# Performance work log

Hardware: AMD Instinct MI355X
Metric: run time of the kernel (lower is better)

The kernel has to match this reference:

```python
import jax, jax.numpy as jnp
import numpy as np

B, E_DIM, N_EXP, EXP_SZ, N_TASKS, TOPK = 16384, 512, 16, 512, 2, 3
D_IN = 2 * E_DIM      # 1024
D_HID = 4 * E_DIM     # 2048
EPS = 1e-5


def _ln(x, g, b):
    mu = jnp.mean(x, axis=-1, keepdims=True)
    var = jnp.var(x, axis=-1, keepdims=True)
    return (x - mu) * jax.lax.rsqrt(var + EPS) * g + b


def setup_inputs() -> dict:
    key = jax.random.key(0)
    ks = jax.random.split(key, 24)
    def w(k, shape, fan_in):
        return jax.random.normal(k, shape, jnp.float32) * (1.0 / np.sqrt(fan_in))
    return {
        "emb_paper": jax.random.normal(ks[0], (B, E_DIM), jnp.float32),
        "emb_reviewer": jax.random.normal(ks[1], (B, E_DIM), jnp.float32),
        # interaction encoder
        "enc_W1": w(ks[2], (D_IN, D_HID), D_IN), "enc_b1": jnp.zeros((D_HID,), jnp.float32),
        "ln1_g": jnp.ones((D_HID,), jnp.float32), "ln1_b": jnp.zeros((D_HID,), jnp.float32),
        "enc_W2": w(ks[3], (D_HID, D_IN), D_HID), "enc_b2": jnp.zeros((D_IN,), jnp.float32),
        "ln2_g": jnp.ones((D_IN,), jnp.float32), "ln2_b": jnp.zeros((D_IN,), jnp.float32),
        # per-task gates (stacked over task axis)
        "gW1": w(ks[4], (N_TASKS, D_IN, 128), D_IN), "gb1": jnp.zeros((N_TASKS, 128), jnp.float32),
        "gW2": w(ks[5], (N_TASKS, 128, N_EXP), 128), "gb2": jnp.zeros((N_TASKS, N_EXP), jnp.float32),
        # stacked experts
        "We1": w(ks[6], (N_EXP, D_IN, EXP_SZ), D_IN), "be1": jnp.zeros((N_EXP, EXP_SZ), jnp.float32),
        "We2": w(ks[7], (N_EXP, EXP_SZ, EXP_SZ), EXP_SZ), "be2": jnp.zeros((N_EXP, EXP_SZ), jnp.float32),
        # per-task towers
        "tW1": w(ks[8], (N_TASKS, EXP_SZ, 256), EXP_SZ), "tb1": jnp.zeros((N_TASKS, 256), jnp.float32),
        "tW2": w(ks[9], (N_TASKS, 256, 128), 256), "tb2": jnp.zeros((N_TASKS, 128), jnp.float32),
        "tW3": w(ks[10], (N_TASKS, 128, 1), 128), "tb3": jnp.zeros((N_TASKS, 1), jnp.float32),
        "task_idx": 0,
    }


def reference(emb_paper, emb_reviewer, enc_W1, enc_b1, ln1_g, ln1_b, enc_W2, enc_b2,
              ln2_g, ln2_b, gW1, gb1, gW2, gb2, We1, be1, We2, be2,
              tW1, tb1, tW2, tb2, tW3, tb3, task_idx):
    # interaction encoder (eval mode: dropout is identity)
    x = jnp.concatenate([emb_paper, emb_reviewer], axis=-1)          # [B, 2E]
    h = jax.nn.relu(_ln(x @ enc_W1 + enc_b1, ln1_g, ln1_b))          # [B, 4E]
    feat = _ln(h @ enc_W2 + enc_b2, ln2_g, ln2_b)                    # [B, 2E]

    # task gate -> top-k sparse softmax gates (no router noise in eval)
    g = jax.nn.relu(feat @ gW1[task_idx] + gb1[task_idx])
    logits = g @ gW2[task_idx] + gb2[task_idx]                       # [B, E]
    top_s, top_i = jax.lax.top_k(logits, TOPK)                       # [B, k]
    gates = jnp.zeros_like(logits).at[jnp.arange(logits.shape[0])[:, None], top_i].set(
        jax.nn.softmax(top_s, axis=-1))

    # dense expert stack (faithful to original: all experts computed)
    e1 = jax.nn.relu(jnp.einsum('bi,eio->beo', feat, We1) + be1[None])   # [B, E, S]
    eo = jnp.einsum('beo,eoh->beh', e1, We2) + be2[None]                 # [B, E, S]
    mix = jnp.einsum('be,beh->bh', gates, eo)                            # [B, S]

    # task tower
    t = jax.nn.relu(mix @ tW1[task_idx] + tb1[task_idx])
    t = jax.nn.relu(t @ tW2[task_idx] + tb2[task_idx])
    out = jax.nn.sigmoid(t @ tW3[task_idx] + tb3[task_idx]).squeeze(-1)  # [B]
    return out, task_idx, gates
```

## Files before the change

kernel.cpp:

```cpp
#include <hip/hip_runtime.h>

typedef __attribute__((ext_vector_type(8))) _Float16 f16x8;
typedef __attribute__((ext_vector_type(4))) float f32x4;

#define DEVINL __device__ __forceinline__

constexpr int BATCH = 16384;
constexpr int DIN   = 1024;
constexpr int DHID  = 2048;
constexpr int NEXP  = 16;
constexpr int EXPSZ = 512;
constexpr int NPAIR = BATCH * 3;

DEVINL unsigned short f2h(float v) {
  _Float16 h = (_Float16)v;
  return __builtin_bit_cast(unsigned short, h);
}
DEVINL float h2f(unsigned short u) {
  return (float)__builtin_bit_cast(_Float16, u);
}

DEVINL void gl2lds(const unsigned short* src, char* ldst) {
  __builtin_amdgcn_global_load_lds((const __attribute__((address_space(1))) void*)src,
                                   (__attribute__((address_space(3))) void*)ldst, 16, 0, 0);
}

template<int SPLIT, int AMODE, int EPI, int BK, int NYT, int TASK>
__global__ __launch_bounds__(256, SPLIT ? 2 : 3)
void mgemm_k(const unsigned short* __restrict__ A0p,
             const unsigned short* __restrict__ A1p,
             const unsigned short* __restrict__ B0p,
             const unsigned short* __restrict__ B1p,
             const float* __restrict__ biasb,
             float* __restrict__ Cf, unsigned short* __restrict__ Cb0,
             unsigned short* __restrict__ Cb1,
             const int* __restrict__ pairRow, const float* __restrict__ pairW,
             const int* __restrict__ counts, const int* __restrict__ offs,
             const int* __restrict__ taskPtr,
             int M, int N, int K)
{
  constexpr int KG = BK / 8;
  constexpr int UNITS = 128 * KG;
  constexpr int ISS = UNITS / 256;
  constexpr int NKK = BK / 32;
  constexpr int NARR = SPLIT ? 4 : 2;
  constexpr bool EXPERT = (AMODE == 1 || AMODE == 2);
  __shared__ char smem[NARR * UNITS * 16];
  char* sA0 = smem;
  char* sA1 = smem + UNITS * 16;
  char* sB0 = smem + (SPLIT ? 2 : 1) * UNITS * 16;
  char* sB1 = smem + 3 * UNITS * 16;

  int Mloc = M, rowBase = 0;
  const unsigned short* b0 = B0p;
  const unsigned short* b1 = B1p;
  const float* bias = biasb;
  if (EXPERT) {
    const int e = blockIdx.z;
    Mloc = counts[e];
    rowBase = offs[e];
    const size_t eo = (size_t)e * (size_t)K * N;
    b0 = B0p + eo;
    if (SPLIT) b1 = B1p + eo;
    bias = biasb + (size_t)e * N;
  }
  if (TASK) bias = biasb + (size_t)(*taskPtr) * N;

  const int xcd = (int)blockIdx.x & 7;
  const int j   = (int)blockIdx.x >> 3;
  const int tile0 = (xcd + 8 * (j / NYT)) * 128;
  const int col0  = (j % NYT) * 128;
  if (tile0 >= Mloc) return;

  const int tid = threadIdx.x;
  const int lane = tid & 63;
  const int wr = ((tid >> 6) >> 1) * 64;
  const int wc = ((tid >> 6) & 1) * 64;
  const int l15 = lane & 15;
  const int lg = lane >> 4;

  const int srow = tid & 127;
  size_t aoff;
  if (AMODE == 0) {
    aoff = (size_t)(tile0 + srow) * K;
  } else if (AMODE == 1) {
    int p = rowBase + tile0 + srow; p = p < NPAIR - 1 ? p : NPAIR - 1;
    aoff = (size_t)pairRow[p] * K;
  } else {
    int p = rowBase + tile0 + srow; p = p < NPAIR - 1 ? p : NPAIR - 1;
    aoff = (size_t)p * K;
  }
  const size_t boff = (size_t)(col0 + srow) * K;

  f32x4 acc[4][4];
  f32x4 acc2[4][4];
  #pragma unroll
  for (int m = 0; m < 4; ++m)
    #pragma unroll
    for (int n = 0; n < 4; ++n) {
      acc[m][n] = f32x4{0.f, 0.f, 0.f, 0.f};
      if (SPLIT) acc2[m][n] = f32x4{0.f, 0.f, 0.f, 0.f};
    }

  for (int kt = 0; kt < K; kt += BK) {
    #pragma unroll
    for (int it = 0; it < ISS; ++it) {
      const int uo = (it * 256 + (tid & 192)) * 16;
      const int ko = kt + (it * 2 + (tid >> 7)) * 8;
      gl2lds(A0p + aoff + ko, sA0 + uo);
      if (SPLIT) gl2lds(A1p + aoff + ko, sA1 + uo);
      gl2lds(b0 + boff + ko, sB0 + uo);
      if (SPLIT) gl2lds(b1 + boff + ko, sB1 + uo);
    }
    __syncthreads();
    #pragma unroll
    for (int kk = 0; kk < NKK; ++kk) {
      const int g = kk * 4 + lg;
      f16x8 b0f[4], b1f[4];
      #pragma unroll
      for (int n = 0; n < 4; ++n) {
        const size_t off = (size_t)(g * 128 + wc + n * 16 + l15) * 16;
        b0f[n] = *(const f16x8*)(sB0 + off);
        if (SPLIT) b1f[n] = *(const f16x8*)(sB1 + off);
      }
      #pragma unroll
      for (int m = 0; m < 4; ++m) {
        const size_t ao = (size_t)(g * 128 + wr + m * 16 + l15) * 16;
        const f16x8 a0 = *(const f16x8*)(sA0 + ao);
        f16x8 a1;
        if (SPLIT) a1 = *(const f16x8*)(sA1 + ao);
        #pragma unroll
        for (int n = 0; n < 4; ++n) {
          if (SPLIT) {
            acc2[m][n] = __builtin_amdgcn_mfma_f32_16x16x32_f16(a1, b0f[n], acc2[m][n], 0, 0, 0);
            acc2[m][n] = __builtin_amdgcn_mfma_f32_16x16x32_f16(a0, b1f[n], acc2[m][n], 0, 0, 0);
          }
          acc[m][n] = __builtin_amdgcn_mfma_f32_16x16x32_f16(a0, b0f[n], acc[m][n], 0, 0, 0);
        }
      }
    }
    __syncthreads();
  }

  #pragma unroll
  for (int n = 0; n < 4; ++n) {
    const int cn = col0 + wc + n * 16 + l15;
    const float bv = bias[cn];
    #pragma unroll
    for (int m = 0; m < 4; ++m) {
      const int r0 = wr + m * 16 + ((lane >> 4) << 2);
      #pragma unroll
      for (int jj = 0; jj < 4; ++jj) {
        const int rm = tile0 + r0 + jj;
        if (EXPERT && rm >= Mloc) continue;
        float v = acc[m][n][jj];
        if (SPLIT) v += acc2[m][n][jj] * (1.f / 2048.f);
        v += bv;
        const size_t ci = (size_t)(EXPERT ? (rowBase + rm) : rm) * N + cn;
        if (EPI == 0) {
          const unsigned short h0 = f2h(v);
          Cb0[ci] = h0;
          Cb1[ci] = f2h((v - h2f(h0)) * 2048.f);
        } else if (EPI == 1) {
          Cb0[ci] = f2h(fmaxf(v, 0.f));
        } else if (EPI == 2) {
          Cb0[ci] = f2h(v * pairW[rowBase + rm]);
        } else {
          Cf[ci] = v;
        }
      }
    }
  }
}

template<bool RELU>
__global__ __launch_bounds__(256, 2)
void gemm32_k(const float* __restrict__ Av, const float* __restrict__ Bb,
              const float* __restrict__ biasb, float* __restrict__ Cv,
              const int* __restrict__ taskPtr, int M, int N, int K)
{
  __shared__ float As[16][128];
  __shared__ float Bs[16][128];
  const int t = *taskPtr;
  const float* Bw = Bb + (size_t)t * K * N;
  const float* bias = biasb + (size_t)t * N;
  const int tile0 = blockIdx.x * 128;
  const int col0 = blockIdx.y * 128;
  const int tid = threadIdx.x;
  const int am = tid >> 1, ak = (tid & 1) * 8;
  const int bk = tid >> 4, bn = (tid & 15) * 8;
  const int rg = (tid >> 4) * 8, cg = (tid & 15) * 8;
  const float* aptr = Av + (size_t)(tile0 + am) * K;

  float acc[8][8];
  #pragma unroll
  for (int i = 0; i < 8; ++i)
    #pragma unroll
    for (int j = 0; j < 8; ++j) acc[i][j] = 0.f;

  for (int kt = 0; kt < K; kt += 16) {
    {
      const float* src = aptr + kt + ak;
      float4 x0 = *reinterpret_cast<const float4*>(src);
      float4 x1 = *reinterpret_cast<const float4*>(src + 4);
      As[ak+0][am]=x0.x; As[ak+1][am]=x0.y; As[ak+2][am]=x0.z; As[ak+3][am]=x0.w;
      As[ak+4][am]=x1.x; As[ak+5][am]=x1.y; As[ak+6][am]=x1.z; As[ak+7][am]=x1.w;
    }
    {
      const float* bsrc = Bw + (size_t)(kt + bk) * N + (col0 + bn);
      float4 b0 = *reinterpret_cast<const float4*>(bsrc);
      float4 b1 = *reinterpret_cast<const float4*>(bsrc + 4);
      Bs[bk][bn+0]=b0.x; Bs[bk][bn+1]=b0.y; Bs[bk][bn+2]=b0.z; Bs[bk][bn+3]=b0.w;
      Bs[bk][bn+4]=b1.x; Bs[bk][bn+5]=b1.y; Bs[bk][bn+6]=b1.z; Bs[bk][bn+7]=b1.w;
    }
    __syncthreads();
    #pragma unroll
    for (int k = 0; k < 16; ++k) {
      float4 a0 = *reinterpret_cast<const float4*>(&As[k][rg]);
      float4 a1 = *reinterpret_cast<const float4*>(&As[k][rg + 4]);
      float4 c0 = *reinterpret_cast<const float4*>(&Bs[k][cg]);
      float4 c1 = *reinterpret_cast<const float4*>(&Bs[k][cg + 4]);
      const float a[8] = {a0.x,a0.y,a0.z,a0.w,a1.x,a1.y,a1.z,a1.w};
      const float b[8] = {c0.x,c0.y,c0.z,c0.w,c1.x,c1.y,c1.z,c1.w};
      #pragma unroll
      for (int i = 0; i < 8; ++i)
        #pragma unroll
        for (int j = 0; j < 8; ++j)
          acc[i][j] = fmaf(a[i], b[j], acc[i][j]);
    }
    __syncthreads();
  }
  #pragma unroll
  for (int i = 0; i < 8; ++i) {
    const int mr = tile0 + rg + i;
    #pragma unroll
    for (int j = 0; j < 8; ++j) {
      float v = acc[i][j] + bias[col0 + cg + j];
      if (RELU) v = fmaxf(v, 0.f);
      Cv[(size_t)mr * N + col0 + cg + j] = v;
    }
  }
}

template<int LEV, int TASK>
__global__ __launch_bounds__(256)
void transp_k(const float* __restrict__ src, unsigned short* __restrict__ d0,
              unsigned short* __restrict__ d1, const int* __restrict__ taskPtr,
              int R, int C)
{
  __shared__ float tle[32][33];
  size_t bb = (size_t)blockIdx.z * R * C;
  if (TASK) bb = (size_t)(*taskPtr) * R * C;
  const int r0 = blockIdx.x * 32, c0 = blockIdx.y * 32;
  const int x = threadIdx.x & 31, y = threadIdx.x >> 5;
  #pragma unroll
  for (int i = 0; i < 32; i += 8)
    tle[y + i][x] = src[bb + (size_t)(r0 + y + i) * C + (c0 + x)];
  __syncthreads();
  const size_t db = TASK ? 0 : (size_t)blockIdx.z * R * C;
  #pragma unroll
  for (int i = 0; i < 32; i += 8) {
    const float v = tle[x][y + i];
    const size_t di = db + (size_t)(c0 + y + i) * R + (r0 + x);
    const unsigned short h0 = f2h(v);
    d0[di] = h0;
    if (LEV > 1) d1[di] = f2h((v - h2f(h0)) * 2048.f);
  }
}

__global__ __launch_bounds__(256)
void convx_k(const float* __restrict__ eP, const float* __restrict__ eR,
             unsigned short* __restrict__ x0, unsigned short* __restrict__ x1)
{
  const size_t u = (size_t)blockIdx.x * 256 + threadIdx.x;
  const size_t row = u >> 8;
  const int c4 = (int)(u & 255) * 4;
  const float* s = (c4 < 512) ? (eP + row * 512 + c4) : (eR + row * 512 + (c4 - 512));
  const float4 v = *(const float4*)s;
  const float vv[4] = {v.x, v.y, v.z, v.w};
  ushort4 h4, l4;
  unsigned short* hp = (unsigned short*)&h4;
  unsigned short* lp = (unsigned short*)&l4;
  #pragma unroll
  for (int j = 0; j < 4; ++j) {
    const unsigned short h0 = f2h(vv[j]);
    hp[j] = h0;
    lp[j] = f2h((vv[j] - h2f(h0)) * 2048.f);
  }
  *(ushort4*)(x0 + row * 1024 + c4) = h4;
  *(ushort4*)(x1 + row * 1024 + c4) = l4;
}

template<int COLS, bool RELU>
__global__ __launch_bounds__(256)
void ln_pair_k(unsigned short* __restrict__ h0, unsigned short* __restrict__ h1,
               const float* __restrict__ g, const float* __restrict__ b)
{
  constexpr int PER = COLS / 256;
  const size_t row = blockIdx.x;
  unsigned short* r0 = h0 + row * COLS;
  unsigned short* r1 = h1 + row * COLS;
  const int c0 = threadIdx.x * PER;
  float v[PER];
  float s = 0.f, s2 = 0.f;
  #pragma unroll
  for (int i = 0; i < PER; i += 4) {
    const ushort4 a = *(const ushort4*)(r0 + c0 + i);
    const ushort4 c = *(const ushort4*)(r1 + c0 + i);
    v[i+0] = h2f(a.x) + h2f(c.x) * (1.f/2048.f);
    v[i+1] = h2f(a.y) + h2f(c.y) * (1.f/2048.f);
    v[i+2] = h2f(a.z) + h2f(c.z) * (1.f/2048.f);
    v[i+3] = h2f(a.w) + h2f(c.w) * (1.f/2048.f);
  }
  #pragma unroll
  for (int i = 0; i < PER; ++i) { s += v[i]; s2 += v[i] * v[i]; }
  #pragma unroll
  for (int o = 1; o < 64; o <<= 1) { s += __shfl_xor(s, o); s2 += __shfl_xor(s2, o); }
  __shared__ float ss[4], ss2[4];
  const int w = threadIdx.x >> 6;
  if ((threadIdx.x & 63) == 0) { ss[w] = s; ss2[w] = s2; }
  __syncthreads();
  s  = ss[0] + ss[1] + ss[2] + ss[3];
  s2 = ss2[0] + ss2[1] + ss2[2] + ss2[3];
  const float mu = s * (1.f / COLS);
  const float var = s2 * (1.f / COLS) - mu * mu;
  const float rs = rsqrtf(var + 1e-5f);
  #pragma unroll
  for (int i = 0; i < PER; i += 4) {
    ushort4 a4, c4v;
    unsigned short* ap = (unsigned short*)&a4;
    unsigned short* cp = (unsigned short*)&c4v;
    #pragma unroll
    for (int j = 0; j < 4; ++j) {
      const int c = c0 + i + j;
      float y = (v[i+j] - mu) * rs * g[c] + b[c];
      if (RELU) y = fmaxf(y, 0.f);
      const unsigned short hh = f2h(y);
      ap[j] = hh;
      cp[j] = f2h((y - h2f(hh)) * 2048.f);
    }
    *(ushort4*)(r0 + c0 + i) = a4;
    *(ushort4*)(r1 + c0 + i) = c4v;
  }
}

template<int COLS, bool RELU, bool F16OUT>
__global__ __launch_bounds__(256)
void ln_k(float* __restrict__ x, const float* __restrict__ g, const float* __restrict__ b,
          unsigned short* __restrict__ x16)
{
  constexpr int PER = COLS / 256;
  const size_t row = blockIdx.x;
  float* xr = x + row * COLS;
  float v[PER];
  float s = 0.f, s2 = 0.f;
  #pragma unroll
  for (int i = 0; i < PER; ++i) {
    v[i] = xr[threadIdx.x + i * 256];
    s += v[i];
    s2 += v[i] * v[i];
  }
  #pragma unroll
  for (int o = 1; o < 64; o <<= 1) { s += __shfl_xor(s, o); s2 += __shfl_xor(s2, o); }
  __shared__ float ss[4], ss2[4];
  const int w = threadIdx.x >> 6;
  if ((threadIdx.x & 63) == 0) { ss[w] = s; ss2[w] = s2; }
  __syncthreads();
  s  = ss[0] + ss[1] + ss[2] + ss[3];
  s2 = ss2[0] + ss2[1] + ss2[2] + ss2[3];
  const float mu = s * (1.f / COLS);
  const float var = s2 * (1.f / COLS) - mu * mu;
  const float rs = rsqrtf(var + 1e-5f);
  #pragma unroll
  for (int i = 0; i < PER; ++i) {
    const int c = threadIdx.x + i * 256;
    float y = (v[i] - mu) * rs * g[c] + b[c];
    if (RELU) y = fmaxf(y, 0.f);
    xr[c] = y;
    if (F16OUT) x16[row * COLS + c] = f2h(y);
  }
}

__global__ __launch_bounds__(256)
void gate_topk_k(const float* __restrict__ g, const float* __restrict__ gW2,
                 const float* __restrict__ gb2, const int* __restrict__ taskPtr,
                 float* __restrict__ gatesOut, int* __restrict__ topkIdx,
                 float* __restrict__ topkW)
{
  const int t = *taskPtr;
  const float* W = gW2 + (size_t)t * 128 * 16;
  const float* bias = gb2 + (size_t)t * 16;
  const int lane = threadIdx.x & 63;
  const int row = blockIdx.x * 4 + (threadIdx.x >> 6);
  const float* gr = g + (size_t)row * 128;
  const int e = lane & 15;
  const int q = lane >> 4;
  float s = 0.f;
  for (int j = q * 32; j < q * 32 + 32; ++j) s = fmaf(gr[j], W[j * 16 + e], s);
  s += __shfl_xor(s, 16);
  s += __shfl_xor(s, 32);
  s += bias[e];
  float logits[16];
  #pragma unroll
  for (int i = 0; i < 16; ++i) logits[i] = __shfl(s, i);
  int i0 = 0; float v0 = logits[0];
  #pragma unroll
  for (int i = 1; i < 16; ++i) if (logits[i] > v0) { v0 = logits[i]; i0 = i; }
  int i1 = -1; float v1 = -3.4e38f;
  #pragma unroll
  for (int i = 0; i < 16; ++i) if (i != i0 && logits[i] > v1) { v1 = logits[i]; i1 = i; }
  int i2 = -1; float v2 = -3.4e38f;
  #pragma unroll
  for (int i = 0; i < 16; ++i) if (i != i0 && i != i1 && logits[i] > v2) { v2 = logits[i]; i2 = i; }
  const float ex1 = expf(v1 - v0);
  const float ex2 = expf(v2 - v0);
  const float inv = 1.f / (1.f + ex1 + ex2);
  const float p0 = inv, p1 = ex1 * inv, p2 = ex2 * inv;
  if (lane < 16) {
    const float gv = (lane == i0) ? p0 : (lane == i1) ? p1 : (lane == i2) ? p2 : 0.f;
    gatesOut[(size_t)row * 16 + lane] = gv;
  }
  if (lane == 0) {
    topkIdx[row * 3 + 0] = i0; topkIdx[row * 3 + 1] = i1; topkIdx[row * 3 + 2] = i2;
    topkW [row * 3 + 0] = p0; topkW [row * 3 + 1] = p1; topkW [row * 3 + 2] = p2;
  }
}

__global__ __launch_bounds__(256)
void hist_k(const int* __restrict__ topkIdx, int* __restrict__ chunkCnt)
{
  __shared__ int lc[NEXP];
  if (threadIdx.x < NEXP) lc[threadIdx.x] = 0;
  __syncthreads();
  const int row = blockIdx.x * 256 + threadIdx.x;
  #pragma unroll
  for (int k = 0; k < 3; ++k) atomicAdd(&lc[topkIdx[row * 3 + k]], 1);
  __syncthreads();
  if (threadIdx.x < NEXP) chunkCnt[blockIdx.x * NEXP + threadIdx.x] = lc[threadIdx.x];
}

__global__ void scanB_k(const int* __restrict__ chunkCnt, int* __restrict__ counts,
                        int* __restrict__ offs, int* __restrict__ chunkBase)
{
  if (threadIdx.x == 0) {
    int tot[NEXP];
    for (int e = 0; e < NEXP; ++e) tot[e] = 0;
    for (int c = 0; c < 64; ++c)
      for (int e = 0; e < NEXP; ++e) tot[e] += chunkCnt[c * NEXP + e];
    int a = 0;
    for (int e = 0; e < NEXP; ++e) { offs[e] = a; counts[e] = tot[e]; a += tot[e]; }
    for (int e = 0; e < NEXP; ++e) {
      int b = offs[e];
      for (int c = 0; c < 64; ++c) { chunkBase[c * NEXP + e] = b; b += chunkCnt[c * NEXP + e]; }
    }
  }
}

__global__ __launch_bounds__(256)
void fill2_k(const int* __restrict__ topkIdx, const float* __restrict__ topkW,
             const int* __restrict__ chunkBase, int* __restrict__ pairRow,
             float* __restrict__ pairW, int* __restrict__ rowPos)
{
  __shared__ int lc[NEXP];
  if (threadIdx.x < NEXP) lc[threadIdx.x] = 0;
  __syncthreads();
  const int row = blockIdx.x * 256 + threadIdx.x;
  #pragma unroll
  for (int k = 0; k < 3; ++k) {
    const int e = topkIdx[row * 3 + k];
    const int lofs = atomicAdd(&lc[e], 1);
    const int pos = chunkBase[blockIdx.x * NEXP + e] + lofs;
    pairRow[pos] = row;
    pairW[pos] = topkW[row * 3 + k];
    rowPos[row * 3 + k] = pos;
  }
}

__global__ __launch_bounds__(256)
void mixreduce_k(const unsigned short* __restrict__ eo, const int* __restrict__ rowPos,
                 unsigned short* __restrict__ mix16)
{
  const size_t row = blockIdx.x;
  const size_t p0 = rowPos[row * 3 + 0];
  const size_t p1 = rowPos[row * 3 + 1];
  const size_t p2 = rowPos[row * 3 + 2];
  for (int c = threadIdx.x; c < EXPSZ; c += 256) {
    mix16[row * EXPSZ + c] = f2h(h2f(eo[p0 * EXPSZ + c]) + h2f(eo[p1 * EXPSZ + c])
                               + h2f(eo[p2 * EXPSZ + c]));
  }
}

__global__ __launch_bounds__(256)
void tower3_k(const unsigned short* __restrict__ t2, const float* __restrict__ tW3,
              const float* __restrict__ tb3, const int* __restrict__ taskPtr,
              float* __restrict__ out)
{
  const int t = *taskPtr;
  const float* w = tW3 + (size_t)t * 128;
  const float bias = tb3[t];
  const int lane = threadIdx.x & 63;
  const int row = blockIdx.x * 4 + (threadIdx.x >> 6);
  const unsigned short* x = t2 + (size_t)row * 128;
  float s = fmaf(h2f(x[lane]), w[lane], h2f(x[lane + 64]) * w[lane + 64]);
  #pragma unroll
  for (int o = 1; o < 64; o <<= 1) s += __shfl_xor(s, o);
  if (lane == 0) out[row] = 1.f / (1.f + expf(-(s + bias)));
  if (blockIdx.x == 0 && threadIdx.x == 0) out[BATCH] = (float)t;
}

extern "C" void kernel_launch(void* const* d_in, const int* in_sizes, int n_in,
                              void* d_out, int out_size, void* d_ws, size_t ws_size,
                              hipStream_t stream)
{
  (void)in_sizes; (void)n_in; (void)out_size; (void)ws_size;
  const float* embP  = (const float*)d_in[0];
  const float* embR  = (const float*)d_in[1];
  const float* encW1 = (const float*)d_in[2];
  const float* encB1 = (const float*)d_in[3];
  const float* ln1g  = (const float*)d_in[4];
  const float* ln1b  = (const float*)d_in[5];
  const float* encW2 = (const float*)d_in[6];
  const float* encB2 = (const float*)d_in[7];
  const float* ln2g  = (const float*)d_in[8];
  const float* ln2b  = (const float*)d_in[9];
  const float* gW1   = (const float*)d_in[10];
  const float* gb1   = (const float*)d_in[11];
  const float* gW2   = (const float*)d_in[12];
  const float* gb2   = (const float*)d_in[13];
  const float* We1   = (const float*)d_in[14];
  const float* be1   = (const float*)d_in[15];
  const float* We2   = (const float*)d_in[16];
  const float* be2   = (const float*)d_in[17];
  const float* tW1   = (const float*)d_in[18];
  const float* tb1   = (const float*)d_in[19];
  const float* tW2   = (const float*)d_in[20];
  const float* tb2   = (const float*)d_in[21];
  const float* tW3   = (const float*)d_in[22];
  const float* tb3   = (const float*)d_in[23];
  const int* taskPtr = (const int*)d_in[24];

  float* out = (float*)d_out;
  char* ws = (char*)d_ws;
  const size_t MB = 1ull << 20;

  unsigned short* x0   = (unsigned short*)(ws);
  unsigned short* x1   = (unsigned short*)(ws + 32 * MB);
  float* feat = (float*)(ws);
  unsigned short* e1b  = (unsigned short*)(ws);
  unsigned short* mix16 = (unsigned short*)(ws);
  unsigned short* t1f16 = (unsigned short*)(ws + 16 * MB);
  unsigned short* t2f16 = (unsigned short*)(ws + 24 * MB);
  unsigned short* h0    = (unsigned short*)(ws + 64 * MB);
  unsigned short* h1    = (unsigned short*)(ws + 128 * MB);
  unsigned short* We1t0 = (unsigned short*)(ws + 64 * MB);
  unsigned short* We2t0 = (unsigned short*)(ws + 80 * MB);
  unsigned short* feat16= (unsigned short*)(ws + 88 * MB);
  unsigned short* eob   = (unsigned short*)(ws + 120 * MB);
  unsigned short* W1t0  = (unsigned short*)(ws + 192 * MB);
  unsigned short* W1t1  = (unsigned short*)(ws + 196 * MB);
  unsigned short* W2t0  = (unsigned short*)(ws + 200 * MB);
  unsigned short* W2t1  = (unsigned short*)(ws + 204 * MB);
  float* gbuf = (float*)(ws + 192 * MB);
  unsigned short* tW1t = (unsigned short*)(ws + 192 * MB);
  unsigned short* tW2t = (unsigned short*)(ws + 193 * MB);
  char* small = ws + 208 * MB;
  int*   counts    = (int*)  (small);
  int*   offs      = (int*)  (small + 1024);
  int*   chunkCnt  = (int*)  (small + 2048);
  int*   chunkBase = (int*)  (small + 2048 + 4096);
  int*   topkIdx   = (int*)  (small + 16384);
  float* topkW     = (float*)(small + 16384 + 196608);
  int*   pairRow   = (int*)  (small + 16384 + 2 * 196608);
  float* pairW     = (float*)(small + 16384 + 3 * 196608);
  int*   rowPos    = (int*)  (small + 16384 + 4 * 196608);

  const dim3 blk(256, 1, 1);

  convx_k<<<dim3(16384, 1, 1), blk, 0, stream>>>(embP, embR, x0, x1);
  transp_k<2,0><<<dim3(DIN/32, DHID/32, 1), blk, 0, stream>>>(encW1, W1t0, W1t1, nullptr, DIN, DHID);
  mgemm_k<1,0,0,32,DHID/128,0><<<dim3((BATCH/128)*(DHID/128), 1, 1), blk, 0, stream>>>(
      x0, x1, W1t0, W1t1, encB1, nullptr, h0, h1,
      nullptr, nullptr, nullptr, nullptr, nullptr, BATCH, DHID, DIN);
  ln_pair_k<DHID, true><<<dim3(BATCH, 1, 1), blk, 0, stream>>>(h0, h1, ln1g, ln1b);

  transp_k<2,0><<<dim3(DHID/32, DIN/32, 1), blk, 0, stream>>>(encW2, W2t0, W2t1, nullptr, DHID, DIN);
  mgemm_k<1,0,3,32,DIN/128,0><<<dim3((BATCH/128)*(DIN/128), 1, 1), blk, 0, stream>>>(
      h0, h1, W2t0, W2t1, encB2, feat, nullptr, nullptr,
      nullptr, nullptr, nullptr, nullptr, nullptr, BATCH, DIN, DHID);
  ln_k<DIN, false, true><<<dim3(BATCH, 1, 1), blk, 0, stream>>>(feat, ln2g, ln2b, feat16);

  gemm32_k<true><<<dim3(BATCH/128, 1, 1), blk, 0, stream>>>(
      feat, gW1, gb1, gbuf, taskPtr, BATCH, 128, DIN);
  gate_topk_k<<<dim3(BATCH/4, 1, 1), blk, 0, stream>>>(
      gbuf, gW2, gb2, taskPtr, out + BATCH + 1, topkIdx, topkW);
  hist_k<<<dim3(BATCH/256, 1, 1), blk, 0, stream>>>(topkIdx, chunkCnt);
  scanB_k<<<dim3(1, 1, 1), dim3(64, 1, 1), 0, stream>>>(chunkCnt, counts, offs, chunkBase);
  fill2_k<<<dim3(BATCH/256, 1, 1), blk, 0, stream>>>(topkIdx, topkW, chunkBase,
                                                     pairRow, pairW, rowPos);

  transp_k<1,0><<<dim3(DIN/32, EXPSZ/32, NEXP), blk, 0, stream>>>(We1, We1t0, nullptr, nullptr, DIN, EXPSZ);
  transp_k<1,0><<<dim3(EXPSZ/32, EXPSZ/32, NEXP), blk, 0, stream>>>(We2, We2t0, nullptr, nullptr, EXPSZ, EXPSZ);

  mgemm_k<0,1,1,64,EXPSZ/128,0><<<dim3((BATCH/128)*(EXPSZ/128), 1, NEXP), blk, 0, stream>>>(
      feat16, nullptr, We1t0, nullptr, be1, nullptr, e1b, nullptr,
      pairRow, nullptr, counts, offs, nullptr, NPAIR, EXPSZ, DIN);
  mgemm_k<0,2,2,64,EXPSZ/128,0><<<dim3((BATCH/128)*(EXPSZ/128), 1, NEXP), blk, 0, stream>>>(
      e1b, nullptr, We2t0, nullptr, be2, nullptr, eob, nullptr,
      nullptr, pairW, counts, offs, nullptr, NPAIR, EXPSZ, EXPSZ);
  mixreduce_k<<<dim3(BATCH, 1, 1), blk, 0, stream>>>(eob, rowPos, mix16);

  transp_k<1,1><<<dim3(EXPSZ/32, 256/32, 1), blk, 0, stream>>>(tW1, tW1t, nullptr, taskPtr, EXPSZ, 256);
  transp_k<1,1><<<dim3(256/32, 128/32, 1), blk, 0, stream>>>(tW2, tW2t, nullptr, taskPtr, 256, 128);
  mgemm_k<0,0,1,64,2,1><<<dim3((BATCH/128)*2, 1, 1), blk, 0, stream>>>(
      mix16, nullptr, tW1t, nullptr, tb1, nullptr, t1f16, nullptr,
      nullptr, nullptr, nullptr, nullptr, taskPtr, BATCH, 256, EXPSZ);
  mgemm_k<0,0,1,64,1,1><<<dim3(BATCH/128, 1, 1), blk, 0, stream>>>(
      t1f16, nullptr, tW2t, nullptr, tb2, nullptr, t2f16, nullptr,
      nullptr, nullptr, nullptr, nullptr, taskPtr, BATCH, 128, 256);
  tower3_k<<<dim3(BATCH/4, 1, 1), blk, 0, stream>>>(t2f16, tW3, tb3, taskPtr, out);
}
```

Measured before the change: 1.218 ms.

## Route gate GEMM through split-fp16 MFMA path and keep feat as fp16 pair

Replaces the fp32 FMA gate GEMM (gemm32_k) with the split-precision MFMA mgemm using a new fused-ReLU fp32 epilogue, fed by a transposed hi/lo fp16 copy of the task's gate weights. The second encoder GEMM now writes feat as an fp16 hi/lo pair, and ln_pair_k replaces the fp32 LayerNorm, so no fp32 feat round trip is needed. The expert GEMM reads feat0 (the hi half) directly. The K tile for the encoder GEMMs also changes from 32 to 64. This trades some precision in the LN2 input and adds a small transpose kernel. Workspace buffers are rearranged to fit the new layout.

```diff
diff --git a/kernel.cpp b/kernel.cpp
--- a/kernel.cpp
+++ b/kernel.cpp
@@ -165,79 +165,12 @@
           Cb0[ci] = f2h(fmaxf(v, 0.f));
         } else if (EPI == 2) {
           Cb0[ci] = f2h(v * pairW[rowBase + rm]);
+        } else if (EPI == 3) {
+          Cf[ci] = v;
         } else {
-          Cf[ci] = v;
+          Cf[ci] = fmaxf(v, 0.f);
         }
       }
-    }
-  }
-}
-
-template<bool RELU>
-__global__ __launch_bounds__(256, 2)
-void gemm32_k(const float* __restrict__ Av, const float* __restrict__ Bb,
-              const float* __restrict__ biasb, float* __restrict__ Cv,
-              const int* __restrict__ taskPtr, int M, int N, int K)
-{
-  __shared__ float As[16][128];
-  __shared__ float Bs[16][128];
-  const int t = *taskPtr;
-  const float* Bw = Bb + (size_t)t * K * N;
-  const float* bias = biasb + (size_t)t * N;
-  const int tile0 = blockIdx.x * 128;
-  const int col0 = blockIdx.y * 128;
-  const int tid = threadIdx.x;
-  const int am = tid >> 1, ak = (tid & 1) * 8;
-  const int bk = tid >> 4, bn = (tid & 15) * 8;
-  const int rg = (tid >> 4) * 8, cg = (tid & 15) * 8;
-  const float* aptr = Av + (size_t)(tile0 + am) * K;
-
-  float acc[8][8];
-  #pragma unroll
-  for (int i = 0; i < 8; ++i)
-    #pragma unroll
-    for (int j = 0; j < 8; ++j) acc[i][j] = 0.f;
-
-  for (int kt = 0; kt < K; kt += 16) {
-    {
-      const float* src = aptr + kt + ak;
-      float4 x0 = *reinterpret_cast<const float4*>(src);
-      float4 x1 = *reinterpret_cast<const float4*>(src + 4);
-      As[ak+0][am]=x0.x; As[ak+1][am]=x0.y; As[ak+2][am]=x0.z; As[ak+3][am]=x0.w;
-      As[ak+4][am]=x1.x; As[ak+5][am]=x1.y; As[ak+6][am]=x1.z; As[ak+7][am]=x1.w;
-    }
-    {
-      const float* bsrc = Bw + (size_t)(kt + bk) * N + (col0 + bn);
-      float4 b0 = *reinterpret_cast<const float4*>(bsrc);
-      float4 b1 = *reinterpret_cast<const float4*>(bsrc + 4);
-      Bs[bk][bn+0]=b0.x; Bs[bk][bn+1]=b0.y; Bs[bk][bn+2]=b0.z; Bs[bk][bn+3]=b0.w;
-      Bs[bk][bn+4]=b1.x; Bs[bk][bn+5]=b1.y; Bs[bk][bn+6]=b1.z; Bs[bk][bn+7]=b1.w;
-    }
-    __syncthreads();
-    #pragma unroll
-    for (int k = 0; k < 16; ++k) {
-      float4 a0 = *reinterpret_cast<const float4*>(&As[k][rg]);
-      float4 a1 = *reinterpret_cast<const float4*>(&As[k][rg + 4]);
-      float4 c0 = *reinterpret_cast<const float4*>(&Bs[k][cg]);
-      float4 c1 = *reinterpret_cast<const float4*>(&Bs[k][cg + 4]);
-      const float a[8] = {a0.x,a0.y,a0.z,a0.w,a1.x,a1.y,a1.z,a1.w};
-      const float b[8] = {c0.x,c0.y,c0.z,c0.w,c1.x,c1.y,c1.z,c1.w};
-      #pragma unroll
-      for (int i = 0; i < 8; ++i)
-        #pragma unroll
-        for (int j = 0; j < 8; ++j)
-          acc[i][j] = fmaf(a[i], b[j], acc[i][j]);
-    }
-    __syncthreads();
-  }
-  #pragma unroll
-  for (int i = 0; i < 8; ++i) {
-    const int mr = tile0 + rg + i;
-    #pragma unroll
-    for (int j = 0; j < 8; ++j) {
-      float v = acc[i][j] + bias[col0 + cg + j];
-      if (RELU) v = fmaxf(v, 0.f);
-      Cv[(size_t)mr * N + col0 + cg + j] = v;
     }
   }
 }
@@ -331,53 +264,16 @@
     unsigned short* ap = (unsigned short*)&a4;
     unsigned short* cp = (unsigned short*)&c4v;
     #pragma unroll
-    for (int j = 0; j < 4; ++j) {
-      const int c = c0 + i + j;
-      float y = (v[i+j] - mu) * rs * g[c] + b[c];
+    for (int jq = 0; jq < 4; ++jq) {
+      const int c = c0 + i + jq;
+      float y = (v[i+jq] - mu) * rs * g[c] + b[c];
       if (RELU) y = fmaxf(y, 0.f);
       const unsigned short hh = f2h(y);
-      ap[j] = hh;
-      cp[j] = f2h((y - h2f(hh)) * 2048.f);
+      ap[jq] = hh;
+      cp[jq] = f2h((y - h2f(hh)) * 2048.f);
     }
     *(ushort4*)(r0 + c0 + i) = a4;
     *(ushort4*)(r1 + c0 + i) = c4v;
-  }
-}
-
-template<int COLS, bool RELU, bool F16OUT>
-__global__ __launch_bounds__(256)
-void ln_k(float* __restrict__ x, const float* __restrict__ g, const float* __restrict__ b,
-          unsigned short* __restrict__ x16)
-{
-  constexpr int PER = COLS / 256;
-  const size_t row = blockIdx.x;
-  float* xr = x + row * COLS;
-  float v[PER];
-  float s = 0.f, s2 = 0.f;
-  #pragma unroll
-  for (int i = 0; i < PER; ++i) {
-    v[i] = xr[threadIdx.x + i * 256];
-    s += v[i];
-    s2 += v[i] * v[i];
-  }
-  #pragma unroll
-  for (int o = 1; o < 64; o <<= 1) { s += __shfl_xor(s, o); s2 += __shfl_xor(s2, o); }
-  __shared__ float ss[4], ss2[4];
-  const int w = threadIdx.x >> 6;
-  if ((threadIdx.x & 63) == 0) { ss[w] = s; ss2[w] = s2; }
-  __syncthreads();
-  s  = ss[0] + ss[1] + ss[2] + ss[3];
-  s2 = ss2[0] + ss2[1] + ss2[2] + ss2[3];
-  const float mu = s * (1.f / COLS);
-  const float var = s2 * (1.f / COLS) - mu * mu;
-  const float rs = rsqrtf(var + 1e-5f);
-  #pragma unroll
-  for (int i = 0; i < PER; ++i) {
-    const int c = threadIdx.x + i * 256;
-    float y = (v[i] - mu) * rs * g[c] + b[c];
-    if (RELU) y = fmaxf(y, 0.f);
-    xr[c] = y;
-    if (F16OUT) x16[row * COLS + c] = f2h(y);
   }
 }
 
@@ -543,23 +439,25 @@
   char* ws = (char*)d_ws;
   const size_t MB = 1ull << 20;
 
-  unsigned short* x0   = (unsigned short*)(ws);
-  unsigned short* x1   = (unsigned short*)(ws + 32 * MB);
-  float* feat = (float*)(ws);
-  unsigned short* e1b  = (unsigned short*)(ws);
-  unsigned short* mix16 = (unsigned short*)(ws);
-  unsigned short* t1f16 = (unsigned short*)(ws + 16 * MB);
-  unsigned short* t2f16 = (unsigned short*)(ws + 24 * MB);
+  unsigned short* x0    = (unsigned short*)(ws);
+  unsigned short* x1    = (unsigned short*)(ws + 32 * MB);
+  unsigned short* feat0 = (unsigned short*)(ws);
+  unsigned short* feat1 = (unsigned short*)(ws + 32 * MB);
+  unsigned short* mix16 = (unsigned short*)(ws + 32 * MB);
+  unsigned short* t1f16 = (unsigned short*)(ws + 48 * MB);
+  unsigned short* t2f16 = (unsigned short*)(ws + 56 * MB);
   unsigned short* h0    = (unsigned short*)(ws + 64 * MB);
   unsigned short* h1    = (unsigned short*)(ws + 128 * MB);
   unsigned short* We1t0 = (unsigned short*)(ws + 64 * MB);
   unsigned short* We2t0 = (unsigned short*)(ws + 80 * MB);
-  unsigned short* feat16= (unsigned short*)(ws + 88 * MB);
-  unsigned short* eob   = (unsigned short*)(ws + 120 * MB);
+  unsigned short* e1b   = (unsigned short*)(ws + 88 * MB);
+  unsigned short* eob   = (unsigned short*)(ws + 136 * MB);
   unsigned short* W1t0  = (unsigned short*)(ws + 192 * MB);
   unsigned short* W1t1  = (unsigned short*)(ws + 196 * MB);
   unsigned short* W2t0  = (unsigned short*)(ws + 200 * MB);
   unsigned short* W2t1  = (unsigned short*)(ws + 204 * MB);
+  unsigned short* gW1t0 = (unsigned short*)(ws + 200 * MB);
+  unsigned short* gW1t1 = (unsigned short*)(ws + 204 * MB);
   float* gbuf = (float*)(ws + 192 * MB);
   unsigned short* tW1t = (unsigned short*)(ws + 192 * MB);
   unsigned short* tW2t = (unsigned short*)(ws + 193 * MB);
@@ -578,19 +476,21 @@
 
   convx_k<<<dim3(16384, 1, 1), blk, 0, stream>>>(embP, embR, x0, x1);
   transp_k<2,0><<<dim3(DIN/32, DHID/32, 1), blk, 0, stream>>>(encW1, W1t0, W1t1, nullptr, DIN, DHID);
-  mgemm_k<1,0,0,32,DHID/128,0><<<dim3((BATCH/128)*(DHID/128), 1, 1), blk, 0, stream>>>(
+  mgemm_k<1,0,0,64,DHID/128,0><<<dim3((BATCH/128)*(DHID/128), 1, 1), blk, 0, stream>>>(
       x0, x1, W1t0, W1t1, encB1, nullptr, h0, h1,
       nullptr, nullptr, nullptr, nullptr, nullptr, BATCH, DHID, DIN);
   ln_pair_k<DHID, true><<<dim3(BATCH, 1, 1), blk, 0, stream>>>(h0, h1, ln1g, ln1b);
 
   transp_k<2,0><<<dim3(DHID/32, DIN/32, 1), blk, 0, stream>>>(encW2, W2t0, W2t1, nullptr, DHID, DIN);
-  mgemm_k<1,0,3,32,DIN/128,0><<<dim3((BATCH/128)*(DIN/128), 1, 1), blk, 0, stream>>>(
-      h0, h1, W2t0, W2t1, encB2, feat, nullptr, nullptr,
+  mgemm_k<1,0,0,64,DIN/128,0><<<dim3((BATCH/128)*(DIN/128), 1, 1), blk, 0, stream>>>(
+      h0, h1, W2t0, W2t1, encB2, nullptr, feat0, feat1,
       nullptr, nullptr, nullptr, nullptr, nullptr, BATCH, DIN, DHID);
-  ln_k<DIN, false, true><<<dim3(BATCH, 1, 1), blk, 0, stream>>>(feat, ln2g, ln2b, feat16);
-
-  gemm32_k<true><<<dim3(BATCH/128, 1, 1), blk, 0, stream>>>(
-      feat, gW1, gb1, gbuf, taskPtr, BATCH, 128, DIN);
+  ln_pair_k<DIN, false><<<dim3(BATCH, 1, 1), blk, 0, stream>>>(feat0, feat1, ln2g, ln2b);
+
+  transp_k<2,1><<<dim3(DIN/32, 128/32, 1), blk, 0, stream>>>(gW1, gW1t0, gW1t1, taskPtr, DIN, 128);
+  mgemm_k<1,0,4,64,1,1><<<dim3(BATCH/128, 1, 1), blk, 0, stream>>>(
+      feat0, feat1, gW1t0, gW1t1, gb1, gbuf, nullptr, nullptr,
+      nullptr, nullptr, nullptr, nullptr, taskPtr, BATCH, 128, DIN);
   gate_topk_k<<<dim3(BATCH/4, 1, 1), blk, 0, stream>>>(
       gbuf, gW2, gb2, taskPtr, out + BATCH + 1, topkIdx, topkW);
   hist_k<<<dim3(BATCH/256, 1, 1), blk, 0, stream>>>(topkIdx, chunkCnt);
@@ -602,7 +502,7 @@
   transp_k<1,0><<<dim3(EXPSZ/32, EXPSZ/32, NEXP), blk, 0, stream>>>(We2, We2t0, nullptr, nullptr, EXPSZ, EXPSZ);
 
   mgemm_k<0,1,1,64,EXPSZ/128,0><<<dim3((BATCH/128)*(EXPSZ/128), 1, NEXP), blk, 0, stream>>>(
-      feat16, nullptr, We1t0, nullptr, be1, nullptr, e1b, nullptr,
+      feat0, nullptr, We1t0, nullptr, be1, nullptr, e1b, nullptr,
       pairRow, nullptr, counts, offs, nullptr, NPAIR, EXPSZ, DIN);
   mgemm_k<0,2,2,64,EXPSZ/128,0><<<dim3((BATCH/128)*(EXPSZ/128), 1, NEXP), blk, 0, stream>>>(
       e1b, nullptr, We2t0, nullptr, be2, nullptr, eob, nullptr,
```

Measured after the change: 1.173 ms. 3.7% less time.
